# Performance work log

Hardware: AMD Instinct MI355X
Metric: run time of the kernel (lower is better)

## Reference

```python
import jax, jax.numpy as jnp
import numpy as np

HEADS = 16

def setup_inputs() -> dict:
    key = jax.random.key(0)
    ks = jax.random.split(key, 5)
    B, N, C = 2, 2048, 1024
    s = 0.02
    return {
        "x": jax.random.normal(ks[0], (B, N, C), jnp.float32),
        "y": jax.random.normal(ks[1], (B, N, C), jnp.float32),
        "w_qkv": jax.random.normal(ks[2], (C, 3 * C), jnp.float32) * s,  # acts as Linear weight^T
        "w_proj": jax.random.normal(ks[3], (C, C), jnp.float32) * s,
        "b_proj": jnp.zeros((C,), jnp.float32),
    }

def _qkv_heads(t, w_qkv, B, N, H, D):
    qkv = (t @ w_qkv).reshape(B, N, 3, H, D)
    qkv = jnp.transpose(qkv, (2, 0, 3, 1, 4))  # [3, B, H, N, D]
    return qkv[0], qkv[1], qkv[2]

def reference(x, y, w_qkv, w_proj, b_proj):
    B, N, C = x.shape
    H = HEADS
    D = C // H
    scale = D ** (-0.5)
    q, k, v = _qkv_heads(x, w_qkv, B, N, H, D)
    q1, k1, v1 = _qkv_heads(y, w_qkv, B, N, H, D)
    attn = jax.nn.softmax(jnp.einsum('bhnd,bhmd->bhnm', q, k) * scale, axis=-1)
    attn1 = jax.nn.softmax(jnp.einsum('bhnd,bhmd->bhnm', q1, k1) * scale, axis=-1)
    # cross-swapped values: x-branch attends over v1 (from y), y-branch over v (from x)
    ox = jnp.einsum('bhnm,bhmd->bhnd', attn, v1)
    oy = jnp.einsum('bhnm,bhmd->bhnd', attn1, v)
    ox = jnp.transpose(ox, (0, 2, 1, 3)).reshape(B, N, C)
    oy = jnp.transpose(oy, (0, 2, 1, 3)).reshape(B, N, C)
    x_out = ox @ w_proj + b_proj + x
    y_out = oy @ w_proj + b_proj + y
    return x_out, y_out
```

## Files before the change

### kernel.cpp

```cpp
#include <hip/hip_runtime.h>

using u16    = unsigned short;
using short8 = __attribute__((ext_vector_type(8))) short;
using f32x4  = __attribute__((ext_vector_type(4))) float;
using f32x16 = __attribute__((ext_vector_type(16))) float;

#define MFMA16(a, b, c) __builtin_amdgcn_mfma_f32_16x16x32_bf16(a, b, c, 0, 0, 0)
#define MFMA32(a, b, c) __builtin_amdgcn_mfma_f32_32x32x16_bf16(a, b, c, 0, 0, 0)

#define QSCALE 0.18033688011112042f

__device__ inline u16 f2bf(float f) {
  union { float f; unsigned u; } v; v.f = f;
  unsigned r = v.u + 0x7fffu + ((v.u >> 16) & 1u);
  return (u16)(r >> 16);
}

__device__ __forceinline__ void load_lds16(const u16* g, u16* l) {
  __builtin_amdgcn_global_load_lds((const __attribute__((address_space(1))) void*)g,
                                   (__attribute__((address_space(3))) void*)l, 16, 0, 0);
}

__global__ __launch_bounds__(256) void cvt_k(const float* __restrict__ src,
                                             u16* __restrict__ dst) {
  const int i = (blockIdx.x * 256 + threadIdx.x) * 8;
  const float4 a = *(const float4*)&src[i];
  const float4 b = *(const float4*)&src[i + 4];
  short8 o;
  o[0] = (short)f2bf(a.x); o[1] = (short)f2bf(a.y);
  o[2] = (short)f2bf(a.z); o[3] = (short)f2bf(a.w);
  o[4] = (short)f2bf(b.x); o[5] = (short)f2bf(b.y);
  o[6] = (short)f2bf(b.z); o[7] = (short)f2bf(b.w);
  *(short8*)&dst[i] = o;
}

__global__ __launch_bounds__(256) void cvtT_k(const float* __restrict__ src,
                                              u16* __restrict__ dst, int R, int C) {
  __shared__ float t[64][65];
  const int c0 = blockIdx.x * 64, r0 = blockIdx.y * 64;
  const int lc = threadIdx.x & 63, g = threadIdx.x >> 6;
#pragma unroll
  for (int i = 0; i < 16; ++i) {
    const int r = g + i * 4;
    t[r][lc] = src[(size_t)(r0 + r) * C + c0 + lc];
  }
  __syncthreads();
#pragma unroll
  for (int i = 0; i < 16; ++i) {
    const int c = g + i * 4;
    dst[(size_t)(c0 + c) * R + r0 + lc] = f2bf(t[lc][c]);
  }
}

template <int MODE>
__global__ __launch_bounds__(256, 2) void gemm_k(
    const u16* __restrict__ A0, const u16* __restrict__ A1,
    const u16* __restrict__ Bt,
    u16* __restrict__ q_out, u16* __restrict__ k_out, u16* __restrict__ v_out,
    float* __restrict__ c0, float* __restrict__ c1,
    const float* __restrict__ bias,
    const float* __restrict__ res0, const float* __restrict__ res1) {
  __shared__ alignas(16) u16 lA[128 * 64];
  __shared__ alignas(16) u16 lB[128 * 64];
  const int z = blockIdx.z;
  const u16* A = z ? A1 : A0;
  float* c_out = z ? c1 : c0;
  const float* res = z ? res1 : res0;
  const int head_base = z * 32;

  const int tid = threadIdx.x;
  const int lane = tid & 63, wave = tid >> 6;
  const int quad = lane >> 4, l16 = lane & 15;
  const int lsw = (l16 & 7) * 8;
  const int wm = (wave >> 1) * 64, wn = (wave & 1) * 64;
  const int bn0 = blockIdx.x * 128, bm0 = blockIdx.y * 128;
  const int srow = lane >> 3;
  const int sg = (lane & 7) ^ srow;

  f32x4 acc[4][4] = {};

  for (int k0 = 0; k0 < 1024; k0 += 64) {
    __syncthreads();
#pragma unroll
    for (int it = 0; it < 4; ++it) {
      const int rb = wave * 32 + it * 8;
      const int r = rb + srow;
      load_lds16(&A[(size_t)(bm0 + r) * 1024 + k0 + sg * 8], &lA[rb * 64]);
      load_lds16(&Bt[(size_t)(bn0 + r) * 1024 + k0 + sg * 8], &lB[rb * 64]);
    }
    asm volatile("s_waitcnt vmcnt(0)" ::: "memory");
    __syncthreads();
#pragma unroll
    for (int kt = 0; kt < 2; ++kt) {
      short8 af[4], bfr[4];
#pragma unroll
      for (int i = 0; i < 4; ++i) {
        const int go = ((kt * 4 + quad) * 8) ^ lsw;
        af[i]  = *(const short8*)&lA[(wm + i * 16 + l16) * 64 + go];
        bfr[i] = *(const short8*)&lB[(wn + i * 16 + l16) * 64 + go];
      }
#pragma unroll
      for (int i = 0; i < 4; ++i)
#pragma unroll
        for (int j = 0; j < 4; ++j)
          acc[i][j] = MFMA16(af[i], bfr[j], acc[i][j]);
    }
  }

#pragma unroll
  for (int i = 0; i < 4; ++i) {
    const int row = bm0 + wm + i * 16 + quad * 4;
#pragma unroll
    for (int j = 0; j < 4; ++j) {
      const int col = bn0 + wn + j * 16 + l16;
#pragma unroll
      for (int r = 0; r < 4; ++r) {
        const float v = acc[i][j][r];
        const int m = row + r;
        if (MODE == 0) {
          const int which = col >> 10;
          const int h = (col >> 6) & 15, d = col & 63;
          const int b = m >> 11, n = m & 2047;
          const size_t hh = (size_t)(head_base + b * 16 + h);
          if (which == 0)      q_out[(hh * 2048 + n) * 64 + d] = f2bf(v * QSCALE);
          else if (which == 1) k_out[(hh * 2048 + n) * 64 + d] = f2bf(v);
          else                 v_out[(hh * 64 + d) * 2048 + n] = f2bf(v);
        } else {
          const size_t idx = (size_t)m * 1024 + col;
          c_out[idx] = v + bias[col] + res[idx];
        }
      }
    }
  }
}

__global__ __launch_bounds__(256, 4) void attn_k(const u16* __restrict__ Q,
                                                 const u16* __restrict__ K,
                                                 const u16* __restrict__ V,
                                                 u16* __restrict__ O) {
  __shared__ alignas(16) u16 kT[64 * 64];
  __shared__ alignas(16) u16 vT[64 * 64];
  __shared__ alignas(16) u16 pT[4][32 * 72];

  const int tid = threadIdx.x;
  const int lane = tid & 63, wave = tid >> 6;
  const int qn = lane & 31, h = lane >> 5;
  const int s = blockIdx.z >> 1, b = blockIdx.z & 1, hh = blockIdx.y;
  const int head_qk = (s * 2 + b) * 16 + hh;
  const int head_v  = ((1 - s) * 2 + b) * 16 + hh;
  const u16* Qh = Q + (size_t)head_qk * 2048 * 64;
  const u16* Kh = K + (size_t)head_qk * 2048 * 64;
  const u16* Vh = V + (size_t)head_v * 64 * 2048;
  const int qr0 = blockIdx.x * 128 + wave * 32;

  short8 qf[4];
#pragma unroll
  for (int f = 0; f < 4; ++f)
    qf[f] = *(const short8*)&Qh[(size_t)(qr0 + qn) * 64 + f * 16 + h * 8];

  f32x16 oacc[2] = {};
  float l_i = 0.f;

  const int srow = lane >> 3;
  const int sg = (lane & 7) ^ srow;

  union PU { uint2 u[2]; short8 s; };

  for (int j0 = 0; j0 < 2048; j0 += 64) {
    __syncthreads();
#pragma unroll
    for (int it = 0; it < 2; ++it) {
      const int rb = wave * 16 + it * 8;
      const int r = rb + srow;
      load_lds16(&Kh[(size_t)(j0 + r) * 64 + sg * 8], &kT[rb * 64]);
      load_lds16(&Vh[(size_t)r * 2048 + j0 + sg * 8], &vT[rb * 64]);
    }
    asm volatile("s_waitcnt vmcnt(0)" ::: "memory");
    __syncthreads();

    f32x16 sacc[2] = {};
#pragma unroll
    for (int t = 0; t < 2; ++t) {
      const int row = t * 32 + qn;
      const int rsw = (row & 7);
#pragma unroll
      for (int kd = 0; kd < 4; ++kd) {
        const int go = ((kd * 2 + h) ^ rsw) * 8;
        const short8 kf = *(const short8*)&kT[row * 64 + go];
        sacc[t] = MFMA32(kf, qf[kd], sacc[t]);
      }
    }

    float p[2][16];
    float rs = 0.f;
#pragma unroll
    for (int t = 0; t < 2; ++t)
#pragma unroll
      for (int r = 0; r < 16; ++r) { p[t][r] = exp2f(sacc[t][r]); rs += p[t][r]; }
    rs += __shfl_xor(rs, 32, 64);
    l_i += rs;

#pragma unroll
    for (int t = 0; t < 2; ++t)
#pragma unroll
      for (int g = 0; g < 4; ++g) {
        const int k0 = 32 * t + 8 * g + 4 * h;
        uint2 w;
        w.x = __builtin_amdgcn_perm(__float_as_uint(p[t][4 * g + 1]),
                                    __float_as_uint(p[t][4 * g + 0]), 0x07060302u);
        w.y = __builtin_amdgcn_perm(__float_as_uint(p[t][4 * g + 3]),
                                    __float_as_uint(p[t][4 * g + 2]), 0x07060302u);
        *(uint2*)&pT[wave][qn * 72 + k0] = w;
      }

    asm volatile("s_waitcnt lgkmcnt(0)" ::: "memory");

    PU pa[4];
#pragma unroll
    for (int st = 0; st < 4; ++st) {
      pa[st].u[0] = *(const uint2*)&pT[wave][qn * 72 + st * 16 + h * 8];
      pa[st].u[1] = *(const uint2*)&pT[wave][qn * 72 + st * 16 + h * 8 + 4];
    }

#pragma unroll
    for (int dt = 0; dt < 2; ++dt) {
      const int row = dt * 32 + qn;
      const int rsw = (row & 7);
#pragma unroll
      for (int st = 0; st < 4; ++st) {
        const int go = ((st * 2 + h) ^ rsw) * 8;
        const short8 vf = *(const short8*)&vT[row * 64 + go];
        oacc[dt] = MFMA32(pa[st].s, vf, oacc[dt]);
      }
    }
  }

  u16* Ob = O + (size_t)s * 4096 * 1024;
#pragma unroll
  for (int r = 0; r < 16; ++r) {
    const int qrow = (r & 3) + 8 * (r >> 2) + 4 * h;
    const float lr = __shfl(l_i, qrow, 64);
    const float inv = 1.f / lr;
    const size_t base = (size_t)(b * 2048 + qr0 + qrow) * 1024 + hh * 64;
#pragma unroll
    for (int dt = 0; dt < 2; ++dt)
      Ob[base + dt * 32 + qn] = f2bf(oacc[dt][r] * inv);
  }
}

extern "C" void kernel_launch(void* const* d_in, const int* in_sizes, int n_in,
                              void* d_out, int out_size, void* d_ws, size_t ws_size,
                              hipStream_t stream) {
  const float* x      = (const float*)d_in[0];
  const float* y      = (const float*)d_in[1];
  const float* w_qkv  = (const float*)d_in[2];
  const float* w_proj = (const float*)d_in[3];
  const float* b_proj = (const float*)d_in[4];
  float* out = (float*)d_out;

  u16* xb     = (u16*)d_ws;
  u16* yb     = xb + 4194304;
  u16* Ob     = xb;
  u16* wqkvT  = yb + 4194304;
  u16* wprojT = wqkvT + 3145728;
  u16* Qs     = wprojT + 1048576;
  u16* Ks     = Qs + 8388608;
  u16* Vs     = Ks + 8388608;

  cvt_k<<<2048, 256, 0, stream>>>(x, xb);
  cvt_k<<<2048, 256, 0, stream>>>(y, yb);
  cvtT_k<<<dim3(48, 16), 256, 0, stream>>>(w_qkv, wqkvT, 1024, 3072);
  cvtT_k<<<dim3(16, 16), 256, 0, stream>>>(w_proj, wprojT, 1024, 1024);

  gemm_k<0><<<dim3(24, 32, 2), 256, 0, stream>>>(xb, yb, wqkvT, Qs, Ks, Vs,
                                                 nullptr, nullptr, nullptr,
                                                 nullptr, nullptr);

  attn_k<<<dim3(16, 16, 4), 256, 0, stream>>>(Qs, Ks, Vs, Ob);

  gemm_k<1><<<dim3(8, 32, 2), 256, 0, stream>>>(Ob, Ob + 4194304, wprojT,
                                                nullptr, nullptr, nullptr,
                                                out, out + 4194304, b_proj, x, y);
}
```

Baseline: 305.8 us.

## Double-buffer LDS in GEMM and attention, keep P in registers via permlane swap

```diff
diff --git a/kernel.cpp b/kernel.cpp
--- a/kernel.cpp
+++ b/kernel.cpp
@@ -19,6 +19,18 @@
 __device__ __forceinline__ void load_lds16(const u16* g, u16* l) {
   __builtin_amdgcn_global_load_lds((const __attribute__((address_space(1))) void*)g,
                                    (__attribute__((address_space(3))) void*)l, 16, 0, 0);
+}
+
+__device__ __forceinline__ unsigned cvt_pk_bf16(float lo, float hi) {
+  unsigned r;
+  asm("v_cvt_pk_bf16_f32 %0, %1, %2" : "=v"(r) : "v"(lo), "v"(hi));
+  return r;
+}
+
+__device__ __forceinline__ void plswap(unsigned& a, unsigned& b) {
+  auto r = __builtin_amdgcn_permlane32_swap(a, b, false, false);
+  a = r[0];
+  b = r[1];
 }
 
 __global__ __launch_bounds__(256) void cvt_k(const float* __restrict__ src,
@@ -60,8 +72,8 @@
     float* __restrict__ c0, float* __restrict__ c1,
     const float* __restrict__ bias,
     const float* __restrict__ res0, const float* __restrict__ res1) {
-  __shared__ alignas(16) u16 lA[128 * 64];
-  __shared__ alignas(16) u16 lB[128 * 64];
+  __shared__ alignas(16) u16 lA[2][128 * 64];
+  __shared__ alignas(16) u16 lB[2][128 * 64];
   const int z = blockIdx.z;
   const u16* A = z ? A1 : A0;
   float* c_out = z ? c1 : c0;
@@ -79,32 +91,43 @@
 
   f32x4 acc[4][4] = {};
 
-  for (int k0 = 0; k0 < 1024; k0 += 64) {
-    __syncthreads();
+  auto gstage = [&](int buf, int k0) {
 #pragma unroll
     for (int it = 0; it < 4; ++it) {
       const int rb = wave * 32 + it * 8;
       const int r = rb + srow;
-      load_lds16(&A[(size_t)(bm0 + r) * 1024 + k0 + sg * 8], &lA[rb * 64]);
-      load_lds16(&Bt[(size_t)(bn0 + r) * 1024 + k0 + sg * 8], &lB[rb * 64]);
+      load_lds16(&A[(size_t)(bm0 + r) * 1024 + k0 + sg * 8], &lA[buf][rb * 64]);
+      load_lds16(&Bt[(size_t)(bn0 + r) * 1024 + k0 + sg * 8], &lB[buf][rb * 64]);
+    }
+  };
+
+  gstage(0, 0);
+  asm volatile("s_waitcnt vmcnt(0)" ::: "memory");
+  __syncthreads();
+
+  int cur = 0;
+  for (int k0 = 0; k0 < 1024; k0 += 64) {
+    if (k0 + 64 < 1024) gstage(cur ^ 1, k0 + 64);
+    const u16* la = lA[cur];
+    const u16* lb = lB[cur];
+#pragma unroll
+    for (int kt = 0; kt < 2; ++kt) {
+      short8 af[4], bfr[4];
+#pragma unroll
+      for (int i = 0; i < 4; ++i) {
+        const int go = ((kt * 4 + quad) * 8) ^ lsw;
+        af[i]  = *(const short8*)&la[(wm + i * 16 + l16) * 64 + go];
+        bfr[i] = *(const short8*)&lb[(wn + i * 16 + l16) * 64 + go];
+      }
+#pragma unroll
+      for (int i = 0; i < 4; ++i)
+#pragma unroll
+        for (int j = 0; j < 4; ++j)
+          acc[i][j] = MFMA16(af[i], bfr[j], acc[i][j]);
     }
     asm volatile("s_waitcnt vmcnt(0)" ::: "memory");
     __syncthreads();
-#pragma unroll
-    for (int kt = 0; kt < 2; ++kt) {
-      short8 af[4], bfr[4];
-#pragma unroll
-      for (int i = 0; i < 4; ++i) {
-        const int go = ((kt * 4 + quad) * 8) ^ lsw;
-        af[i]  = *(const short8*)&lA[(wm + i * 16 + l16) * 64 + go];
-        bfr[i] = *(const short8*)&lB[(wn + i * 16 + l16) * 64 + go];
-      }
-#pragma unroll
-      for (int i = 0; i < 4; ++i)
-#pragma unroll
-        for (int j = 0; j < 4; ++j)
-          acc[i][j] = MFMA16(af[i], bfr[j], acc[i][j]);
-    }
+    cur ^= 1;
   }
 
 #pragma unroll
@@ -138,9 +161,8 @@
                                                  const u16* __restrict__ K,
                                                  const u16* __restrict__ V,
                                                  u16* __restrict__ O) {
-  __shared__ alignas(16) u16 kT[64 * 64];
-  __shared__ alignas(16) u16 vT[64 * 64];
-  __shared__ alignas(16) u16 pT[4][32 * 72];
+  __shared__ alignas(16) u16 kT[2][64 * 64];
+  __shared__ alignas(16) u16 vT[2][64 * 64];
 
   const int tid = threadIdx.x;
   const int lane = tid & 63, wave = tid >> 6;
@@ -164,21 +186,30 @@
   const int srow = lane >> 3;
   const int sg = (lane & 7) ^ srow;
 
-  union PU { uint2 u[2]; short8 s; };
-
-  for (int j0 = 0; j0 < 2048; j0 += 64) {
-    __syncthreads();
+  union PU { unsigned u[4]; short8 s; };
+
+  auto stage = [&](int buf, int j0) {
 #pragma unroll
     for (int it = 0; it < 2; ++it) {
       const int rb = wave * 16 + it * 8;
       const int r = rb + srow;
-      load_lds16(&Kh[(size_t)(j0 + r) * 64 + sg * 8], &kT[rb * 64]);
-      load_lds16(&Vh[(size_t)r * 2048 + j0 + sg * 8], &vT[rb * 64]);
-    }
-    asm volatile("s_waitcnt vmcnt(0)" ::: "memory");
-    __syncthreads();
+      load_lds16(&Kh[(size_t)(j0 + r) * 64 + sg * 8], &kT[buf][rb * 64]);
+      load_lds16(&Vh[(size_t)r * 2048 + j0 + sg * 8], &vT[buf][rb * 64]);
+    }
+  };
+
+  stage(0, 0);
+  asm volatile("s_waitcnt vmcnt(0)" ::: "memory");
+  __syncthreads();
+
+  int cur = 0;
+  for (int j0 = 0; j0 < 2048; j0 += 64) {
+    if (j0 + 64 < 2048) stage(cur ^ 1, j0 + 64);
+    const u16* kb = kT[cur];
+    const u16* vb = vT[cur];
 
     f32x16 sacc[2] = {};
+    __builtin_amdgcn_s_setprio(1);
 #pragma unroll
     for (int t = 0; t < 2; ++t) {
       const int row = t * 32 + qn;
@@ -186,42 +217,41 @@
 #pragma unroll
       for (int kd = 0; kd < 4; ++kd) {
         const int go = ((kd * 2 + h) ^ rsw) * 8;
-        const short8 kf = *(const short8*)&kT[row * 64 + go];
+        const short8 kf = *(const short8*)&kb[row * 64 + go];
         sacc[t] = MFMA32(kf, qf[kd], sacc[t]);
       }
     }
-
-    float p[2][16];
+    __builtin_amdgcn_s_setprio(0);
+
     float rs = 0.f;
+    unsigned pw[2][8];
 #pragma unroll
     for (int t = 0; t < 2; ++t)
 #pragma unroll
-      for (int r = 0; r < 16; ++r) { p[t][r] = exp2f(sacc[t][r]); rs += p[t][r]; }
+      for (int j = 0; j < 8; ++j) {
+        const float pa0 = exp2f(sacc[t][2 * j]);
+        const float pa1 = exp2f(sacc[t][2 * j + 1]);
+        rs += pa0 + pa1;
+        pw[t][j] = cvt_pk_bf16(pa0, pa1);
+      }
+
+    PU pa[4];
+#pragma unroll
+    for (int t = 0; t < 2; ++t)
+#pragma unroll
+      for (int e = 0; e < 2; ++e) {
+        unsigned a0 = pw[t][4 * e + 0], a2 = pw[t][4 * e + 2];
+        unsigned a1 = pw[t][4 * e + 1], a3 = pw[t][4 * e + 3];
+        plswap(a0, a2);
+        plswap(a1, a3);
+        pa[2 * t + e].u[0] = a0; pa[2 * t + e].u[1] = a1;
+        pa[2 * t + e].u[2] = a2; pa[2 * t + e].u[3] = a3;
+      }
+
     rs += __shfl_xor(rs, 32, 64);
     l_i += rs;
 
-#pragma unroll
-    for (int t = 0; t < 2; ++t)
-#pragma unroll
-      for (int g = 0; g < 4; ++g) {
-        const int k0 = 32 * t + 8 * g + 4 * h;
-        uint2 w;
-        w.x = __builtin_amdgcn_perm(__float_as_uint(p[t][4 * g + 1]),
-                                    __float_as_uint(p[t][4 * g + 0]), 0x07060302u);
-        w.y = __builtin_amdgcn_perm(__float_as_uint(p[t][4 * g + 3]),
-                                    __float_as_uint(p[t][4 * g + 2]), 0x07060302u);
-        *(uint2*)&pT[wave][qn * 72 + k0] = w;
-      }
-
-    asm volatile("s_waitcnt lgkmcnt(0)" ::: "memory");
-
-    PU pa[4];
-#pragma unroll
-    for (int st = 0; st < 4; ++st) {
-      pa[st].u[0] = *(const uint2*)&pT[wave][qn * 72 + st * 16 + h * 8];
-      pa[st].u[1] = *(const uint2*)&pT[wave][qn * 72 + st * 16 + h * 8 + 4];
-    }
-
+    __builtin_amdgcn_s_setprio(1);
 #pragma unroll
     for (int dt = 0; dt < 2; ++dt) {
       const int row = dt * 32 + qn;
@@ -229,10 +259,15 @@
 #pragma unroll
       for (int st = 0; st < 4; ++st) {
         const int go = ((st * 2 + h) ^ rsw) * 8;
-        const short8 vf = *(const short8*)&vT[row * 64 + go];
+        const short8 vf = *(const short8*)&vb[row * 64 + go];
         oacc[dt] = MFMA32(pa[st].s, vf, oacc[dt]);
       }
     }
+    __builtin_amdgcn_s_setprio(0);
+
+    asm volatile("s_waitcnt vmcnt(0)" ::: "memory");
+    __syncthreads();
+    cur ^= 1;
   }
 
   u16* Ob = O + (size_t)s * 4096 * 1024;
```

New measurement: 325.6 us. 6.5% more time.
